# Performance work log

Measured on AMD Instinct MI355X. Metric: run time of the kernel, lower is better.

Reference implementation:

```python
import jax, jax.numpy as jnp
import numpy as np

N_NODES = 50000
N_EDGES = 800000
F_IN, HID, N_CLS = 128, 64, 40


def gcn_conv(x, edge_index, W, b):
    """PyG GCNConv: add self-loops, symmetric normalization, linear, aggregate, bias."""
    n = x.shape[0]
    loop = jnp.arange(n, dtype=edge_index.dtype)
    src = jnp.concatenate([edge_index[0], loop])  # [E+N]
    dst = jnp.concatenate([edge_index[1], loop])  # [E+N]
    deg = jax.ops.segment_sum(jnp.ones_like(dst, dtype=x.dtype), dst, num_segments=n)
    dinv = jnp.where(deg > 0, jax.lax.rsqrt(deg), 0.0)
    norm = dinv[src] * dinv[dst]                   # [E+N]
    h = x @ W                                      # [N, out]
    out = jax.ops.segment_sum(h[src] * norm[:, None], dst, num_segments=n)
    return out + b


def setup_inputs() -> dict:
    key = jax.random.key(0)
    k1, k2, k3, k4 = jax.random.split(key, 4)
    x = jax.random.normal(k1, (N_NODES, F_IN), dtype=jnp.float32)
    edge_index = jax.random.randint(k2, (2, N_EDGES), 0, N_NODES, dtype=jnp.int32)
    W1 = jax.random.normal(k3, (F_IN, HID), dtype=jnp.float32) / np.sqrt(F_IN)
    b1 = jnp.zeros((HID,), dtype=jnp.float32)
    W2 = jax.random.normal(k4, (HID, N_CLS), dtype=jnp.float32) / np.sqrt(HID)
    b2 = jnp.zeros((N_CLS,), dtype=jnp.float32)
    return {"x": x, "edge_index": edge_index, "W1": W1, "b1": b1, "W2": W2, "b2": b2}


def reference(x, edge_index, W1, b1, W2, b2):
    # layer 1: GCNConv -> ReLU -> Dropout(eval = identity)
    h = jax.nn.relu(gcn_conv(x, edge_index, W1, b1))
    # layer 2: GCNConv -> ReLU -> Dropout(eval = identity); return_logits=True
    h = jax.nn.relu(gcn_conv(h, edge_index, W2, b2))
    return h
```

## Files before the change

kernel.cpp:

```cpp
#include <hip/hip_runtime.h>
#include <hip/hip_bf16.h>
#include <hip/hip_fp16.h>


#define N_FEAT_IN 128
#define N_HID 64
#define N_CLS 40
#define CAP 64

__device__ __forceinline__ void h8_acc(uint4 u, float4& a0, float4& a1) {
    __half2* h = (__half2*)&u;
    float2 f0 = __half22float2(h[0]);
    float2 f1 = __half22float2(h[1]);
    float2 f2 = __half22float2(h[2]);
    float2 f3 = __half22float2(h[3]);
    a0.x += f0.x; a0.y += f0.y; a0.z += f1.x; a0.w += f1.y;
    a1.x += f2.x; a1.y += f2.y; a1.z += f3.x; a1.w += f3.y;
}

__device__ __forceinline__ uint4 f8_to_h8(float4 a0, float4 a1) {
    uint4 u;
    ((__half2*)&u)[0] = __floats2half2_rn(a0.x, a0.y);
    ((__half2*)&u)[1] = __floats2half2_rn(a0.z, a0.w);
    ((__half2*)&u)[2] = __floats2half2_rn(a1.x, a1.y);
    ((__half2*)&u)[3] = __floats2half2_rn(a1.z, a1.w);
    return u;
}

__device__ __forceinline__ uint2 f4_to_h4(float4 v) {
    uint2 w;
    *(__half2*)&w.x = __floats2half2_rn(v.x, v.y);
    *(__half2*)&w.y = __floats2half2_rn(v.z, v.w);
    return w;
}

__global__ __launch_bounds__(256) void k_g1c(
    const float* __restrict__ x, const float* __restrict__ W,
    __half* __restrict__ h1u, int n, int gb,
    const int* __restrict__ ei, int* deg, int* __restrict__ rank, int E) {
    __shared__ float Wl[64 * 64];
    __shared__ float Xs[64 * 68];
    int t = threadIdx.x;
    if (blockIdx.x >= gb) {
        int e0 = (blockIdx.x - gb) * 1024 + t;
#pragma unroll
        for (int q = 0; q < 4; ++q) {
            int e = e0 + q * 256;
            if (e < E) {
                int d = ei[E + e];
                rank[e] = atomicAdd(&deg[d], 1);
            }
        }
        return;
    }
    int node0 = blockIdx.x * 64;
    int tn = t & 15;
    int tc = t >> 4;
    float acc[4][4] = {};
    for (int p = 0; p < 2; ++p) {
#pragma unroll
        for (int i = 0; i < 4; ++i) {
            int r = (t >> 4) + 16 * i;
            int c4 = t & 15;
            *(float4*)&Wl[r * 64 + c4 * 4] =
                *(const float4*)&W[(p * 64 + r) * N_HID + c4 * 4];
            int gr = node0 + r;
            float4 v = (gr < n)
                ? *(const float4*)&x[(size_t)gr * N_FEAT_IN + p * 64 + c4 * 4]
                : make_float4(0.f, 0.f, 0.f, 0.f);
            *(float4*)&Xs[r * 68 + c4 * 4] = v;
        }
        __syncthreads();
        for (int k = 0; k < 64; k += 4) {
            float4 xa[4], wb[4];
#pragma unroll
            for (int i = 0; i < 4; ++i)
                xa[i] = *(float4*)&Xs[(tn + 16 * i) * 68 + k];
#pragma unroll
            for (int kk = 0; kk < 4; ++kk)
                wb[kk] = *(float4*)&Wl[(k + kk) * 64 + tc * 4];
#pragma unroll
            for (int kk = 0; kk < 4; ++kk)
#pragma unroll
                for (int i = 0; i < 4; ++i)
#pragma unroll
                    for (int j = 0; j < 4; ++j)
                        acc[i][j] += ((const float*)&xa[i])[kk] * ((const float*)&wb[kk])[j];
        }
        __syncthreads();
    }
#pragma unroll
    for (int i = 0; i < 4; ++i) {
        int gr = node0 + tn + 16 * i;
        if (gr < n) {
            float4 v = make_float4(acc[i][0], acc[i][1], acc[i][2], acc[i][3]);
            *(uint2*)(h1u + (size_t)gr * N_HID + tc * 4) = f4_to_h4(v);
        }
    }
}

__global__ __launch_bounds__(256) void k_scat(
    const int* __restrict__ ei, const int* __restrict__ rank,
    unsigned short* __restrict__ csr, int E, int cb,
    const int* __restrict__ deg, __half* __restrict__ h1u, int n) {
    if (blockIdx.x < cb) {
        int e = blockIdx.x * blockDim.x + threadIdx.x;
        if (e >= E) return;
        int s = ei[e];
        int d = ei[E + e];
        int r = rank[e];
        if (r < CAP) csr[(d << 6) + r] = (unsigned short)s;
        return;
    }
    int i = (blockIdx.x - cb) * 256 + threadIdx.x;
    if (i >= n * 8) return;
    int node = i >> 3;
    float din = 1.0f / sqrtf((float)(deg[node] + 1));
    uint4 u = ((uint4*)h1u)[i];
    __half2* h = (__half2*)&u;
    float2 f0 = __half22float2(h[0]);
    float2 f1 = __half22float2(h[1]);
    float2 f2 = __half22float2(h[2]);
    float2 f3 = __half22float2(h[3]);
    float4 a0 = make_float4(din * f0.x, din * f0.y, din * f1.x, din * f1.y);
    float4 a1 = make_float4(din * f2.x, din * f2.y, din * f3.x, din * f3.y);
    ((uint4*)h1u)[i] = f8_to_h8(a0, a1);
}

template <bool L1>
__global__ __launch_bounds__(256) void k_aggrh(const int* __restrict__ dgi,
                                               const unsigned short* __restrict__ csr,
                                               const __half* __restrict__ hs,
                                               const float* __restrict__ b,
                                               __half* __restrict__ outp, int n) {
    __shared__ int Ss[4][2][32];
    int wv = threadIdx.x >> 6, lane = threadIdx.x & 63;
    int hf = lane >> 5;
    int hl = lane & 31;
    int g = hl >> 3;
    int l8 = hl & 7;
    int node = blockIdx.x * 8 + wv * 2 + hf;
    bool active = node < n;
    float4 a0 = make_float4(0.f, 0.f, 0.f, 0.f);
    float4 a1 = make_float4(0.f, 0.f, 0.f, 0.f);
    int dn = 0;
    if (active) dn = dgi[node];
    int cap = min(dn, CAP);
    float din = active ? 1.0f / sqrtf((float)(dn + 1)) : 0.f;
    if (active && g == 0) {
        uint4 u = *(const uint4*)(hs + ((size_t)node << 6) + l8 * 8);
        h8_acc(u, a0, a1);
    }
    const int base = node << 6;
    for (int j0 = 0; j0 < cap; j0 += 32) {
        int j = j0 + hl;
        if (j < cap) Ss[wv][hf][hl] = (int)csr[base + j];
        int cnt = min(32, cap - j0);
        int t = 0;
        for (; t + 16 <= cnt; t += 16) {
            int s1 = Ss[wv][hf][t + g];
            int s2 = Ss[wv][hf][t + 4 + g];
            int s3 = Ss[wv][hf][t + 8 + g];
            int s4 = Ss[wv][hf][t + 12 + g];
            uint4 u1 = *(const uint4*)(hs + ((size_t)s1 << 6) + l8 * 8);
            uint4 u2 = *(const uint4*)(hs + ((size_t)s2 << 6) + l8 * 8);
            uint4 u3 = *(const uint4*)(hs + ((size_t)s3 << 6) + l8 * 8);
            uint4 u4 = *(const uint4*)(hs + ((size_t)s4 << 6) + l8 * 8);
            h8_acc(u1, a0, a1);
            h8_acc(u2, a0, a1);
            h8_acc(u3, a0, a1);
            h8_acc(u4, a0, a1);
        }
        if (t + 8 <= cnt) {
            int s1 = Ss[wv][hf][t + g];
            int s2 = Ss[wv][hf][t + 4 + g];
            uint4 u1 = *(const uint4*)(hs + ((size_t)s1 << 6) + l8 * 8);
            uint4 u2 = *(const uint4*)(hs + ((size_t)s2 << 6) + l8 * 8);
            h8_acc(u1, a0, a1);
            h8_acc(u2, a0, a1);
            t += 8;
        }
        for (; t < cnt; t += 4) {
            int e = t + g;
            if (e < cnt) {
                int s = Ss[wv][hf][e];
                uint4 u = *(const uint4*)(hs + ((size_t)s << 6) + l8 * 8);
                h8_acc(u, a0, a1);
            }
        }
    }
    a0.x += __shfl_xor(a0.x, 8);  a0.y += __shfl_xor(a0.y, 8);
    a0.z += __shfl_xor(a0.z, 8);  a0.w += __shfl_xor(a0.w, 8);
    a1.x += __shfl_xor(a1.x, 8);  a1.y += __shfl_xor(a1.y, 8);
    a1.z += __shfl_xor(a1.z, 8);  a1.w += __shfl_xor(a1.w, 8);
    a0.x += __shfl_xor(a0.x, 16); a0.y += __shfl_xor(a0.y, 16);
    a0.z += __shfl_xor(a0.z, 16); a0.w += __shfl_xor(a0.w, 16);
    a1.x += __shfl_xor(a1.x, 16); a1.y += __shfl_xor(a1.y, 16);
    a1.z += __shfl_xor(a1.z, 16); a1.w += __shfl_xor(a1.w, 16);
    if (active && g == 0) {
        float4 o0, o1;
        if (L1) {
            float4 b0 = *(const float4*)&b[l8 * 8];
            float4 b1 = *(const float4*)&b[l8 * 8 + 4];
            o0.x = fmaxf(din * a0.x + b0.x, 0.f) * din;
            o0.y = fmaxf(din * a0.y + b0.y, 0.f) * din;
            o0.z = fmaxf(din * a0.z + b0.z, 0.f) * din;
            o0.w = fmaxf(din * a0.w + b0.w, 0.f) * din;
            o1.x = fmaxf(din * a1.x + b1.x, 0.f) * din;
            o1.y = fmaxf(din * a1.y + b1.y, 0.f) * din;
            o1.z = fmaxf(din * a1.z + b1.z, 0.f) * din;
            o1.w = fmaxf(din * a1.w + b1.w, 0.f) * din;
        } else {
            o0 = make_float4(din * a0.x, din * a0.y, din * a0.z, din * a0.w);
            o1 = make_float4(din * a1.x, din * a1.y, din * a1.z, din * a1.w);
        }
        *(uint4*)(outp + ((size_t)node << 6) + l8 * 8) = f8_to_h8(o0, o1);
    }
}

__global__ __launch_bounds__(256, 2) void k_gemm2f(const __half* __restrict__ g2,
                                                   const float* __restrict__ W,
                                                   const float* __restrict__ bias,
                                                   float* __restrict__ out, int n) {
    __shared__ float Wl[N_HID * N_CLS];
    __shared__ float Xs[64 * 68];
    int t = threadIdx.x;
    int node0 = blockIdx.x * 64;
    for (int i = t * 4; i < N_HID * N_CLS; i += 1024)
        *(float4*)&Wl[i] = *(const float4*)&W[i];
#pragma unroll
    for (int q = 0; q < 2; ++q) {
        int idx = q * 256 + t;
        int r = idx >> 3, c8 = idx & 7;
        int gr = node0 + r;
        uint4 u = make_uint4(0u, 0u, 0u, 0u);
        if (gr < n) u = *(const uint4*)(g2 + (size_t)gr * N_HID + c8 * 8);
        __half2* h = (__half2*)&u;
        float2 f0 = __half22float2(h[0]);
        float2 f1 = __half22float2(h[1]);
        float2 f2 = __half22float2(h[2]);
        float2 f3 = __half22float2(h[3]);
        float* xp = &Xs[r * 68 + c8 * 8];
        *(float4*)&xp[0] = make_float4(f0.x, f0.y, f1.x, f1.y);
        *(float4*)&xp[4] = make_float4(f2.x, f2.y, f3.x, f3.y);
    }
    __syncthreads();
    int tn = t & 15;
    int tc = t >> 4;
    if (tc < 10) {
        float acc[4][4] = {};
        for (int k = 0; k < N_HID; k += 4) {
            float4 xa[4], wb[4];
#pragma unroll
            for (int i = 0; i < 4; ++i)
                xa[i] = *(float4*)&Xs[(tn + 16 * i) * 68 + k];
#pragma unroll
            for (int kk = 0; kk < 4; ++kk)
                wb[kk] = *(float4*)&Wl[(k + kk) * N_CLS + tc * 4];
#pragma unroll
            for (int kk = 0; kk < 4; ++kk)
#pragma unroll
                for (int i = 0; i < 4; ++i)
#pragma unroll
                    for (int j = 0; j < 4; ++j)
                        acc[i][j] += ((const float*)&xa[i])[kk] * ((const float*)&wb[kk])[j];
        }
        float4 bv = *(const float4*)&bias[tc * 4];
#pragma unroll
        for (int i = 0; i < 4; ++i) {
            int gr = node0 + tn + 16 * i;
            if (gr < n) {
                float4 v = make_float4(fmaxf(acc[i][0] + bv.x, 0.f),
                                       fmaxf(acc[i][1] + bv.y, 0.f),
                                       fmaxf(acc[i][2] + bv.z, 0.f),
                                       fmaxf(acc[i][3] + bv.w, 0.f));
                *(float4*)&out[(size_t)gr * N_CLS + tc * 4] = v;
            }
        }
    }
}

extern "C" void kernel_launch(void* const* d_in, const int* in_sizes, int n_in,
                              void* d_out, int out_size, void* d_ws, size_t ws_size,
                              hipStream_t stream) {
    const float* x = (const float*)d_in[0];
    const int* ei = (const int*)d_in[1];
    const float* W1 = (const float*)d_in[2];
    const float* b1 = (const float*)d_in[3];
    const float* W2 = (const float*)d_in[4];
    const float* b2 = (const float*)d_in[5];
    float* out = (float*)d_out;

    int n = in_sizes[0] / N_FEAT_IN;
    int E = in_sizes[1] / 2;

    char* ws = (char*)d_ws;
    int*            deg_i = (int*)           (ws + 0);
    int*            rank  = (int*)           (ws + 200704);
    unsigned short* csr   = (unsigned short*)(ws + 3400704);
    __half*         h1u   = (__half*)        (ws + 9800704);
    __half*         out1s = (__half*)        (ws + 16200704);
    __half*         g2h   = h1u;

    int gb = (n + 63) / 64;
    int cb = (E + 255) / 256;
    int cb4 = (E + 1023) / 1024;
    int sb = (n * 8 + 255) / 256;

    hipMemsetAsync(deg_i, 0, (size_t)n * sizeof(int), stream);
    k_g1c<<<gb + cb4, 256, 0, stream>>>(x, W1, h1u, n, gb, ei, deg_i, rank, E);
    k_scat<<<cb + sb, 256, 0, stream>>>(ei, rank, csr, E, cb, deg_i, h1u, n);

    k_aggrh<true><<<(n + 7) / 8, 256, 0, stream>>>(deg_i, csr, h1u,
                                                   b1, out1s, n);
    k_aggrh<false><<<(n + 7) / 8, 256, 0, stream>>>(deg_i, csr, out1s,
                                                    nullptr, g2h, n);
    k_gemm2f<<<gb, 256, 0, stream>>>(g2h, W2, b2, out, n);
}
```

Measured before the change: 104.5 us.

## Fuse second-layer aggregation with the W2 GEMM, bias and ReLU

The second aggregation kernel and the separate W2 GEMM kernel are merged into one kernel. Each half-wave aggregates a node's neighbours, writes the normalized 64-wide row to shared memory, then computes the 40 outputs against W2 staged in LDS. This removes one launch and the fp16 round trip of the intermediate through global memory. In exchange, every block reloads W2 into LDS, and the per-node matvec runs on lanes that are partly idle (only 8 lanes compute the second column group).

```diff
diff --git a/kernel.cpp b/kernel.cpp
--- a/kernel.cpp
+++ b/kernel.cpp
@@ -127,8 +127,7 @@
     ((uint4*)h1u)[i] = f8_to_h8(a0, a1);
 }
 
-template <bool L1>
-__global__ __launch_bounds__(256) void k_aggrh(const int* __restrict__ dgi,
+__global__ __launch_bounds__(256) void k_aggr1(const int* __restrict__ dgi,
                                                const unsigned short* __restrict__ csr,
                                                const __half* __restrict__ hs,
                                                const float* __restrict__ b,
@@ -198,86 +197,117 @@
     a1.x += __shfl_xor(a1.x, 16); a1.y += __shfl_xor(a1.y, 16);
     a1.z += __shfl_xor(a1.z, 16); a1.w += __shfl_xor(a1.w, 16);
     if (active && g == 0) {
+        float4 b0 = *(const float4*)&b[l8 * 8];
+        float4 b1 = *(const float4*)&b[l8 * 8 + 4];
         float4 o0, o1;
-        if (L1) {
-            float4 b0 = *(const float4*)&b[l8 * 8];
-            float4 b1 = *(const float4*)&b[l8 * 8 + 4];
-            o0.x = fmaxf(din * a0.x + b0.x, 0.f) * din;
-            o0.y = fmaxf(din * a0.y + b0.y, 0.f) * din;
-            o0.z = fmaxf(din * a0.z + b0.z, 0.f) * din;
-            o0.w = fmaxf(din * a0.w + b0.w, 0.f) * din;
-            o1.x = fmaxf(din * a1.x + b1.x, 0.f) * din;
-            o1.y = fmaxf(din * a1.y + b1.y, 0.f) * din;
-            o1.z = fmaxf(din * a1.z + b1.z, 0.f) * din;
-            o1.w = fmaxf(din * a1.w + b1.w, 0.f) * din;
-        } else {
-            o0 = make_float4(din * a0.x, din * a0.y, din * a0.z, din * a0.w);
-            o1 = make_float4(din * a1.x, din * a1.y, din * a1.z, din * a1.w);
-        }
+        o0.x = fmaxf(din * a0.x + b0.x, 0.f) * din;
+        o0.y = fmaxf(din * a0.y + b0.y, 0.f) * din;
+        o0.z = fmaxf(din * a0.z + b0.z, 0.f) * din;
+        o0.w = fmaxf(din * a0.w + b0.w, 0.f) * din;
+        o1.x = fmaxf(din * a1.x + b1.x, 0.f) * din;
+        o1.y = fmaxf(din * a1.y + b1.y, 0.f) * din;
+        o1.z = fmaxf(din * a1.z + b1.z, 0.f) * din;
+        o1.w = fmaxf(din * a1.w + b1.w, 0.f) * din;
         *(uint4*)(outp + ((size_t)node << 6) + l8 * 8) = f8_to_h8(o0, o1);
     }
 }
 
-__global__ __launch_bounds__(256, 2) void k_gemm2f(const __half* __restrict__ g2,
-                                                   const float* __restrict__ W,
-                                                   const float* __restrict__ bias,
-                                                   float* __restrict__ out, int n) {
-    __shared__ float Wl[N_HID * N_CLS];
-    __shared__ float Xs[64 * 68];
+__global__ __launch_bounds__(256) void k_aggr2g(const int* __restrict__ dgi,
+                                                const unsigned short* __restrict__ csr,
+                                                const __half* __restrict__ hs,
+                                                const float* __restrict__ W2,
+                                                const float* __restrict__ b2,
+                                                float* __restrict__ out, int n) {
+    __shared__ float W2l[N_HID * N_CLS];
+    __shared__ int Ss[4][2][32];
+    __shared__ float Rw[4][2][N_HID];
     int t = threadIdx.x;
-    int node0 = blockIdx.x * 64;
     for (int i = t * 4; i < N_HID * N_CLS; i += 1024)
-        *(float4*)&Wl[i] = *(const float4*)&W[i];
-#pragma unroll
-    for (int q = 0; q < 2; ++q) {
-        int idx = q * 256 + t;
-        int r = idx >> 3, c8 = idx & 7;
-        int gr = node0 + r;
-        uint4 u = make_uint4(0u, 0u, 0u, 0u);
-        if (gr < n) u = *(const uint4*)(g2 + (size_t)gr * N_HID + c8 * 8);
-        __half2* h = (__half2*)&u;
-        float2 f0 = __half22float2(h[0]);
-        float2 f1 = __half22float2(h[1]);
-        float2 f2 = __half22float2(h[2]);
-        float2 f3 = __half22float2(h[3]);
-        float* xp = &Xs[r * 68 + c8 * 8];
-        *(float4*)&xp[0] = make_float4(f0.x, f0.y, f1.x, f1.y);
-        *(float4*)&xp[4] = make_float4(f2.x, f2.y, f3.x, f3.y);
-    }
+        *(float4*)&W2l[i] = *(const float4*)&W2[i];
     __syncthreads();
-    int tn = t & 15;
-    int tc = t >> 4;
-    if (tc < 10) {
-        float acc[4][4] = {};
-        for (int k = 0; k < N_HID; k += 4) {
-            float4 xa[4], wb[4];
-#pragma unroll
-            for (int i = 0; i < 4; ++i)
-                xa[i] = *(float4*)&Xs[(tn + 16 * i) * 68 + k];
-#pragma unroll
-            for (int kk = 0; kk < 4; ++kk)
-                wb[kk] = *(float4*)&Wl[(k + kk) * N_CLS + tc * 4];
-#pragma unroll
-            for (int kk = 0; kk < 4; ++kk)
-#pragma unroll
-                for (int i = 0; i < 4; ++i)
-#pragma unroll
-                    for (int j = 0; j < 4; ++j)
-                        acc[i][j] += ((const float*)&xa[i])[kk] * ((const float*)&wb[kk])[j];
-        }
-        float4 bv = *(const float4*)&bias[tc * 4];
-#pragma unroll
-        for (int i = 0; i < 4; ++i) {
-            int gr = node0 + tn + 16 * i;
-            if (gr < n) {
-                float4 v = make_float4(fmaxf(acc[i][0] + bv.x, 0.f),
-                                       fmaxf(acc[i][1] + bv.y, 0.f),
-                                       fmaxf(acc[i][2] + bv.z, 0.f),
-                                       fmaxf(acc[i][3] + bv.w, 0.f));
-                *(float4*)&out[(size_t)gr * N_CLS + tc * 4] = v;
+    int wv = t >> 6, lane = t & 63;
+    int hf = lane >> 5;
+    int hl = lane & 31;
+    int g = hl >> 3;
+    int l8 = hl & 7;
+    int node = blockIdx.x * 8 + wv * 2 + hf;
+    bool active = node < n;
+    float4 a0 = make_float4(0.f, 0.f, 0.f, 0.f);
+    float4 a1 = make_float4(0.f, 0.f, 0.f, 0.f);
+    int dn = 0;
+    if (active) dn = dgi[node];
+    int cap = min(dn, CAP);
+    float din = active ? 1.0f / sqrtf((float)(dn + 1)) : 0.f;
+    if (active && g == 0) {
+        uint4 u = *(const uint4*)(hs + ((size_t)node << 6) + l8 * 8);
+        h8_acc(u, a0, a1);
+    }
+    const int base = node << 6;
+    for (int j0 = 0; j0 < cap; j0 += 32) {
+        int j = j0 + hl;
+        if (j < cap) Ss[wv][hf][hl] = (int)csr[base + j];
+        int cnt = min(32, cap - j0);
+        int t2 = 0;
+        for (; t2 + 16 <= cnt; t2 += 16) {
+            int s1 = Ss[wv][hf][t2 + g];
+            int s2 = Ss[wv][hf][t2 + 4 + g];
+            int s3 = Ss[wv][hf][t2 + 8 + g];
+            int s4 = Ss[wv][hf][t2 + 12 + g];
+            uint4 u1 = *(const uint4*)(hs + ((size_t)s1 << 6) + l8 * 8);
+            uint4 u2 = *(const uint4*)(hs + ((size_t)s2 << 6) + l8 * 8);
+            uint4 u3 = *(const uint4*)(hs + ((size_t)s3 << 6) + l8 * 8);
+            uint4 u4 = *(const uint4*)(hs + ((size_t)s4 << 6) + l8 * 8);
+            h8_acc(u1, a0, a1);
+            h8_acc(u2, a0, a1);
+            h8_acc(u3, a0, a1);
+            h8_acc(u4, a0, a1);
+        }
+        if (t2 + 8 <= cnt) {
+            int s1 = Ss[wv][hf][t2 + g];
+            int s2 = Ss[wv][hf][t2 + 4 + g];
+            uint4 u1 = *(const uint4*)(hs + ((size_t)s1 << 6) + l8 * 8);
+            uint4 u2 = *(const uint4*)(hs + ((size_t)s2 << 6) + l8 * 8);
+            h8_acc(u1, a0, a1);
+            h8_acc(u2, a0, a1);
+            t2 += 8;
+        }
+        for (; t2 < cnt; t2 += 4) {
+            int e = t2 + g;
+            if (e < cnt) {
+                int s = Ss[wv][hf][e];
+                uint4 u = *(const uint4*)(hs + ((size_t)s << 6) + l8 * 8);
+                h8_acc(u, a0, a1);
             }
         }
     }
+    a0.x += __shfl_xor(a0.x, 8);  a0.y += __shfl_xor(a0.y, 8);
+    a0.z += __shfl_xor(a0.z, 8);  a0.w += __shfl_xor(a0.w, 8);
+    a1.x += __shfl_xor(a1.x, 8);  a1.y += __shfl_xor(a1.y, 8);
+    a1.z += __shfl_xor(a1.z, 8);  a1.w += __shfl_xor(a1.w, 8);
+    a0.x += __shfl_xor(a0.x, 16); a0.y += __shfl_xor(a0.y, 16);
+    a0.z += __shfl_xor(a0.z, 16); a0.w += __shfl_xor(a0.w, 16);
+    a1.x += __shfl_xor(a1.x, 16); a1.y += __shfl_xor(a1.y, 16);
+    a1.z += __shfl_xor(a1.z, 16); a1.w += __shfl_xor(a1.w, 16);
+    if (!active) return;
+    if (g == 0) {
+        float* rp = &Rw[wv][hf][l8 * 8];
+        *(float4*)&rp[0] = make_float4(din * a0.x, din * a0.y, din * a0.z, din * a0.w);
+        *(float4*)&rp[4] = make_float4(din * a1.x, din * a1.y, din * a1.z, din * a1.w);
+    }
+    const float* row = Rw[wv][hf];
+    int c1 = hl;
+    int c2 = 32 + hl;
+    float o1 = b2[c1];
+    float o2 = (hl < 8) ? b2[c2] : 0.f;
+#pragma unroll 8
+    for (int k = 0; k < N_HID; ++k) {
+        float rv = row[k];
+        o1 += rv * W2l[k * N_CLS + c1];
+        if (hl < 8) o2 += rv * W2l[k * N_CLS + c2];
+    }
+    float* op = out + (size_t)node * N_CLS;
+    op[c1] = fmaxf(o1, 0.f);
+    if (hl < 8) op[c2] = fmaxf(o2, 0.f);
 }
 
 extern "C" void kernel_launch(void* const* d_in, const int* in_sizes, int n_in,
@@ -300,7 +330,6 @@
     unsigned short* csr   = (unsigned short*)(ws + 3400704);
     __half*         h1u   = (__half*)        (ws + 9800704);
     __half*         out1s = (__half*)        (ws + 16200704);
-    __half*         g2h   = h1u;
 
     int gb = (n + 63) / 64;
     int cb = (E + 255) / 256;
@@ -311,9 +340,6 @@
     k_g1c<<<gb + cb4, 256, 0, stream>>>(x, W1, h1u, n, gb, ei, deg_i, rank, E);
     k_scat<<<cb + sb, 256, 0, stream>>>(ei, rank, csr, E, cb, deg_i, h1u, n);
 
-    k_aggrh<true><<<(n + 7) / 8, 256, 0, stream>>>(deg_i, csr, h1u,
-                                                   b1, out1s, n);
-    k_aggrh<false><<<(n + 7) / 8, 256, 0, stream>>>(deg_i, csr, out1s,
-                                                    nullptr, g2h, n);
-    k_gemm2f<<<gb, 256, 0, stream>>>(g2h, W2, b2, out, n);
-}
+    k_aggr1<<<(n + 7) / 8, 256, 0, stream>>>(deg_i, csr, h1u, b1, out1s, n);
+    k_aggr2g<<<(n + 7) / 8, 256, 0, stream>>>(deg_i, csr, out1s, W2, b2, out, n);
+}
```

After: 112.0 us. 1.07x slower.
